# Optimization experiments

Measured on AMD Instinct MI355X. Metric: run time of the kernel, lower is better.

The kernel has to match this reference:

```python
import jax, jax.numpy as jnp
import numpy as np

N_LANGS = 2
VOCAB = 200000
DIM = 300
B = 1024
S = 50
EPS = 1e-5  # BatchNorm1d default eps


def _bn(x):
    # BatchNorm1d(affine=False) in training mode: per-batch stats, biased variance
    return (x - x.mean(axis=0)) / jnp.sqrt(x.var(axis=0) + EPS)


def setup_inputs() -> dict:
    key = jax.random.key(0)
    ks = jax.random.split(key, 16)
    # frozen per-language embedding tables, stacked: [n_langs, vocab, dim]
    tables = jax.random.normal(ks[0], (N_LANGS, VOCAB, DIM), jnp.float32) * 0.1
    tables = tables.at[:, 0, :].set(0.0)  # padding_idx=0 row
    langs_1 = jax.random.randint(ks[1], (B,), 0, N_LANGS, dtype=jnp.int32)
    langs_2 = jax.random.randint(ks[2], (B,), 0, N_LANGS, dtype=jnp.int32)
    sents_1 = jax.random.randint(ks[3], (B, S), 0, VOCAB, dtype=jnp.int64)
    sents_2 = jax.random.randint(ks[4], (B, S), 0, VOCAB, dtype=jnp.int64)
    # lin1/lin2 initialized to identity in the original module
    w1 = jnp.eye(DIM, dtype=jnp.float32)
    b1 = jax.random.uniform(ks[5], (DIM,), jnp.float32, -0.05, 0.05)
    w2 = jnp.eye(DIM, dtype=jnp.float32)
    b2 = jax.random.uniform(ks[6], (DIM,), jnp.float32, -0.05, 0.05)
    w3 = jax.random.normal(ks[7], (400, 901), jnp.float32) * 0.03
    b3 = jax.random.uniform(ks[8], (400,), jnp.float32, -0.03, 0.03)
    w4 = jax.random.normal(ks[9], (100, 400), jnp.float32) * 0.05
    b4 = jax.random.uniform(ks[10], (100,), jnp.float32, -0.05, 0.05)
    w5 = jax.random.normal(ks[11], (1, 100), jnp.float32) * 0.1
    b5 = jax.random.uniform(ks[12], (1,), jnp.float32, -0.1, 0.1)
    return {
        "langs_1": langs_1, "sents_1": sents_1,
        "langs_2": langs_2, "sents_2": sents_2,
        "tables": tables,
        "w1": w1, "b1": b1, "w2": w2, "b2": b2,
        "w3": w3, "b3": b3, "w4": w4, "b4": b4,
        "w5": w5, "b5": b5,
    }


def reference(langs_1, sents_1, langs_2, sents_2, tables,
              w1, b1, w2, b2, w3, b3, w4, b4, w5, b5):
    # batched table-select + embedding lookup + sum-pool (replaces the per-sample loop)
    x1 = tables[langs_1[:, None], sents_1].sum(axis=1)  # [B, 300]
    x2 = tables[langs_2[:, None], sents_2].sum(axis=1)  # [B, 300]

    def enc(x):
        h = jax.nn.relu(_bn(x @ w1.T + b1))
        return jax.nn.relu(_bn(h @ w2.T + b2))

    o1 = enc(x1)
    o2 = enc(x2)
    cor = jnp.sum(o1 * o2, axis=1, keepdims=True)          # [B, 1]
    nxt = jnp.concatenate([o1, o2, jnp.abs(o1 - o2), cor], axis=1)  # [B, 901]
    h = jax.nn.relu(_bn(nxt @ w3.T + b3))                  # [B, 400]
    h = jax.nn.relu(_bn(h @ w4.T + b4))                    # [B, 100]
    score = h @ w5.T + b5                                  # [B, 1]
    prob = jax.nn.sigmoid(score)
    return prob, o1, o2
```

## Files before the change

kernel.cpp:

```cpp
#include <hip/hip_runtime.h>
#include <math.h>

#define EPS 1e-5f
#define INV_N (1.0f / 1024.0f)


typedef _Float16 f16x8 __attribute__((ext_vector_type(8)));
typedef float f32x4 __attribute__((ext_vector_type(4)));

__device__ __forceinline__ _Float16 f2h(float f) { return (_Float16)f; }

static const int STATS_TOTAL = 3400;

__global__ __launch_bounds__(128) void gather_kernel(
    const int* __restrict__ langs1, const int* __restrict__ sents1,
    const int* __restrict__ langs2, const int* __restrict__ sents2,
    const float* __restrict__ tables, _Float16* __restrict__ xb,
    float* __restrict__ stats)
{
    int idx = blockIdx.x, t = threadIdx.x;
    if (idx == 0) {
        for (int i = t; i < STATS_TOTAL; i += 128) stats[i] = 0.f;
    }
    int side = idx >> 10, b = idx & 1023;
    const int* langs = side ? langs2 : langs1;
    const int* sents = side ? sents2 : sents1;
    __shared__ int toks[50];
    if (t < 50) toks[t] = sents[b * 50 + t];
    __syncthreads();
    const float* base = tables + (size_t)langs[b] * (200000ull * 300ull);
    float a0 = 0.f, a1 = 0.f, a2 = 0.f;
    #pragma unroll 5
    for (int s = 0; s < 50; s++) {
        const float* row = base + (size_t)toks[s] * 300;
        a0 += row[t];
        a1 += row[t + 128];
        if (t < 44) a2 += row[t + 256];
    }
    _Float16* xr = xb + (size_t)idx * 320;
    xr[t] = f2h(a0);
    xr[t + 128] = f2h(a1);
    if (t < 64) xr[t + 256] = (t < 44) ? f2h(a2) : (_Float16)0.f;
}

__global__ __launch_bounds__(256) void wcvt_kernel(
    const float* __restrict__ w1, const float* __restrict__ w2,
    const float* __restrict__ w3, const float* __restrict__ w4,
    _Float16* __restrict__ w1b, _Float16* __restrict__ w2b,
    _Float16* __restrict__ w3b, _Float16* __restrict__ w4b)
{
    int i = blockIdx.x * 256 + threadIdx.x;
    if (i < 102400) {
        int r = i / 320, c = i - r * 320;
        w1b[i] = (r < 300 && c < 300) ? f2h(w1[r * 300 + c]) : (_Float16)0.f;
    } else if (i < 204800) {
        int j = i - 102400; int r = j / 320, c = j - r * 320;
        w2b[j] = (r < 300 && c < 300) ? f2h(w2[r * 300 + c]) : (_Float16)0.f;
    } else if (i < 620544) {
        int j = i - 204800; int r = j / 928, c = j - r * 928;
        w3b[j] = (r < 400 && c < 901) ? f2h(w3[r * 901 + c]) : (_Float16)0.f;
    } else if (i < 673792) {
        int j = i - 620544; int r = j / 416, c = j - r * 416;
        w4b[j] = (r < 100 && c < 400) ? f2h(w4[r * 400 + c]) : (_Float16)0.f;
    }
}

__global__ __launch_bounds__(256) void gemm_f16(
    const _Float16* __restrict__ A, const _Float16* __restrict__ W, int ldk,
    const float* __restrict__ bias, float* __restrict__ C, int ldc,
    int N, int kIters, float* __restrict__ sSum, float* __restrict__ sSq,
    int twoSided)
{
    __shared__ __align__(16) _Float16 lsA[2048];
    __shared__ __align__(16) _Float16 lsW[2048];
    int tid = threadIdx.x;
    int r0 = blockIdx.x * 64, c0 = blockIdx.y * 64;
    int lane = tid & 63;
    int wave = tid >> 6;
    int waveR = wave & 1, waveC = wave >> 1;
    int q = lane >> 4, m = lane & 15;

    int srow = tid >> 2, sseg = tid & 3;
    const _Float16* gA = A + (size_t)(r0 + srow) * ldk + sseg * 8;
    const _Float16* gW = W + (size_t)(c0 + srow) * ldk + sseg * 8;
    _Float16* stA = &lsA[sseg * 512 + srow * 8];
    _Float16* stW = &lsW[sseg * 512 + srow * 8];

    int aoff0 = q * 512 + (waveR * 32 + m) * 8;
    int aoff1 = aoff0 + 128;
    int boff0 = q * 512 + (waveC * 32 + m) * 8;
    int boff1 = boff0 + 128;

    f32x4 acc00 = {0.f,0.f,0.f,0.f}, acc01 = {0.f,0.f,0.f,0.f};
    f32x4 acc10 = {0.f,0.f,0.f,0.f}, acc11 = {0.f,0.f,0.f,0.f};

    for (int kt = 0; kt < kIters; kt++) {
        uint4 va = *(const uint4*)gA;
        uint4 vw = *(const uint4*)gW;
        gA += 32; gW += 32;
        __syncthreads();
        *(uint4*)stA = va;
        *(uint4*)stW = vw;
        __syncthreads();
        f16x8 a0 = *(const f16x8*)&lsA[aoff0];
        f16x8 a1 = *(const f16x8*)&lsA[aoff1];
        f16x8 b0 = *(const f16x8*)&lsW[boff0];
        f16x8 b1 = *(const f16x8*)&lsW[boff1];
        acc00 = __builtin_amdgcn_mfma_f32_16x16x32_f16(a0, b0, acc00, 0, 0, 0);
        acc01 = __builtin_amdgcn_mfma_f32_16x16x32_f16(a0, b1, acc01, 0, 0, 0);
        acc10 = __builtin_amdgcn_mfma_f32_16x16x32_f16(a1, b0, acc10, 0, 0, 0);
        acc11 = __builtin_amdgcn_mfma_f32_16x16x32_f16(a1, b1, acc11, 0, 0, 0);
    }

    int side = (twoSided && r0 >= 1024) ? 1 : 0;
    int gc0 = c0 + waveC * 32 + m;
    int gc1 = gc0 + 16;
    float bias0 = (gc0 < N) ? bias[gc0] : 0.f;
    float bias1 = (gc1 < N) ? bias[gc1] : 0.f;
    float colS0 = 0.f, colQ0 = 0.f, colS1 = 0.f, colQ1 = 0.f;
    #pragma unroll
    for (int i = 0; i < 2; i++) {
        f32x4 cv0 = i ? acc10 : acc00;
        f32x4 cv1 = i ? acc11 : acc01;
        #pragma unroll
        for (int r = 0; r < 4; r++) {
            int gr = r0 + waveR * 32 + i * 16 + q * 4 + r;
            if (gc0 < N) {
                float v = cv0[r] + bias0;
                C[(size_t)gr * ldc + gc0] = v;
                colS0 += v; colQ0 += v * v;
            }
            if (gc1 < N) {
                float v = cv1[r] + bias1;
                C[(size_t)gr * ldc + gc1] = v;
                colS1 += v; colQ1 += v * v;
            }
        }
    }
    colS0 += __shfl_down(colS0, 32); colS0 += __shfl_down(colS0, 16);
    colQ0 += __shfl_down(colQ0, 32); colQ0 += __shfl_down(colQ0, 16);
    colS1 += __shfl_down(colS1, 32); colS1 += __shfl_down(colS1, 16);
    colQ1 += __shfl_down(colQ1, 32); colQ1 += __shfl_down(colQ1, 16);
    if (q == 0) {
        if (gc0 < N) {
            atomicAdd(&sSum[side * N + gc0], colS0);
            atomicAdd(&sSq[side * N + gc0], colQ0);
        }
        if (gc1 < N) {
            atomicAdd(&sSum[side * N + gc1], colS1);
            atomicAdd(&sSq[side * N + gc1], colQ1);
        }
    }
}

__global__ __launch_bounds__(256) void bncvt1_kernel(
    const float* __restrict__ z, const float* __restrict__ sS,
    const float* __restrict__ sQ, _Float16* __restrict__ out)
{
    int i = blockIdx.x * 256 + threadIdx.x;
    int r = i / 320, c = i - r * 320;
    _Float16 v = (_Float16)0.f;
    if (c < 300) {
        int side = r >> 10;
        float mean = sS[side * 300 + c] * INV_N;
        float var  = sQ[side * 300 + c] * INV_N - mean * mean;
        float x = (z[r * 300 + c] - mean) * rsqrtf(var + EPS);
        v = f2h(fmaxf(x, 0.f));
    }
    out[i] = v;
}

__global__ __launch_bounds__(256) void bncvt3_kernel(
    const float* __restrict__ z, const float* __restrict__ sS,
    const float* __restrict__ sQ, _Float16* __restrict__ out)
{
    int i = blockIdx.x * 256 + threadIdx.x;
    int r = i / 416, c = i - r * 416;
    _Float16 v = (_Float16)0.f;
    if (c < 400) {
        float mean = sS[c] * INV_N;
        float var  = sQ[c] * INV_N - mean * mean;
        float x = (z[r * 400 + c] - mean) * rsqrtf(var + EPS);
        v = f2h(fmaxf(x, 0.f));
    }
    out[i] = v;
}

__global__ __launch_bounds__(128) void pair_kernel(
    const float* __restrict__ z2, const float* __restrict__ sS,
    const float* __restrict__ sQ, float* __restrict__ out,
    _Float16* __restrict__ nxtb)
{
    int b = blockIdx.x, t = threadIdx.x;
    __shared__ float red[128];
    float dot = 0.f;
    for (int d = t; d < 300; d += 128) {
        float m1 = sS[d] * INV_N;
        float v1 = sQ[d] * INV_N - m1 * m1;
        float m2 = sS[300 + d] * INV_N;
        float v2 = sQ[300 + d] * INV_N - m2 * m2;
        float a1 = fmaxf((z2[(size_t)b * 300 + d] - m1) * rsqrtf(v1 + EPS), 0.f);
        float a2 = fmaxf((z2[(size_t)(1024 + b) * 300 + d] - m2) * rsqrtf(v2 + EPS), 0.f);
        out[1024 + (size_t)b * 300 + d] = a1;
        out[308224 + (size_t)b * 300 + d] = a2;
        nxtb[(size_t)b * 928 + d] = f2h(a1);
        nxtb[(size_t)b * 928 + 300 + d] = f2h(a2);
        nxtb[(size_t)b * 928 + 600 + d] = f2h(fabsf(a1 - a2));
        dot += a1 * a2;
    }
    red[t] = dot;
    __syncthreads();
    if (t < 27) nxtb[(size_t)b * 928 + 901 + t] = (_Float16)0.f;
    if (t == 0) {
        float s = 0.f;
        for (int i = 0; i < 128; i++) s += red[i];
        nxtb[(size_t)b * 928 + 900] = f2h(s);
    }
}

__global__ __launch_bounds__(64) void final_kernel(
    const float* __restrict__ y4, const float* __restrict__ sS,
    const float* __restrict__ sQ, const float* __restrict__ w5,
    const float* __restrict__ b5, float* __restrict__ out)
{
    int b = blockIdx.x, l = threadIdx.x;
    float acc = 0.f;
    for (int j = l; j < 100; j += 64) {
        float mean = sS[j] * INV_N;
        float var = sQ[j] * INV_N - mean * mean;
        float v = (y4[(size_t)b * 100 + j] - mean) * rsqrtf(var + EPS);
        v = v > 0.f ? v : 0.f;
        acc += v * w5[j];
    }
    #pragma unroll
    for (int off = 32; off; off >>= 1) acc += __shfl_down(acc, off);
    if (l == 0) out[b] = 1.f / (1.f + expf(-(acc + b5[0])));
}

extern "C" void kernel_launch(void* const* d_in, const int* in_sizes, int n_in,
                              void* d_out, int out_size, void* d_ws, size_t ws_size,
                              hipStream_t stream)
{
    const int* langs1 = (const int*)d_in[0];
    const int* sents1 = (const int*)d_in[1];
    const int* langs2 = (const int*)d_in[2];
    const int* sents2 = (const int*)d_in[3];
    const float* tables = (const float*)d_in[4];
    const float* w1 = (const float*)d_in[5];
    const float* b1 = (const float*)d_in[6];
    const float* w2 = (const float*)d_in[7];
    const float* b2 = (const float*)d_in[8];
    const float* w3 = (const float*)d_in[9];
    const float* b3 = (const float*)d_in[10];
    const float* w4 = (const float*)d_in[11];
    const float* b4 = (const float*)d_in[12];
    const float* w5 = (const float*)d_in[13];
    const float* b5 = (const float*)d_in[14];

    float* ws = (float*)d_ws;
    float* F0 = ws;
    float* F1 = ws + 614400;
    float* stats = ws + 1228800;
    float* s1S = stats;        float* s1Q = stats + 600;
    float* s2S = stats + 1200; float* s2Q = stats + 1800;
    float* s3S = stats + 2400; float* s3Q = stats + 2800;
    float* s4S = stats + 3200; float* s4Q = stats + 3300;
    _Float16* hb = (_Float16*)(ws + 1232208);
    _Float16* xb   = hb;
    _Float16* a1b  = hb + 655360;
    _Float16* nxtb = hb + 1310720;
    _Float16* a3b  = hb + 2260992;
    _Float16* w1b  = hb + 2686976;
    _Float16* w2b  = hb + 2789376;
    _Float16* w3b  = hb + 2891776;
    _Float16* w4b  = hb + 3307520;

    float* out = (float*)d_out;

    gather_kernel<<<2048, 128, 0, stream>>>(langs1, sents1, langs2, sents2,
                                            tables, xb, stats);
    wcvt_kernel<<<2632, 256, 0, stream>>>(w1, w2, w3, w4, w1b, w2b, w3b, w4b);
    gemm_f16<<<dim3(32, 5), 256, 0, stream>>>(xb, w1b, 320, b1, F0, 300,
                                              300, 10, s1S, s1Q, 1);
    bncvt1_kernel<<<2560, 256, 0, stream>>>(F0, s1S, s1Q, a1b);
    gemm_f16<<<dim3(32, 5), 256, 0, stream>>>(a1b, w2b, 320, b2, F1, 300,
                                              300, 10, s2S, s2Q, 1);
    pair_kernel<<<1024, 128, 0, stream>>>(F1, s2S, s2Q, out, nxtb);
    gemm_f16<<<dim3(16, 7), 256, 0, stream>>>(nxtb, w3b, 928, b3, F0, 400,
                                              400, 29, s3S, s3Q, 0);
    bncvt3_kernel<<<1664, 256, 0, stream>>>(F0, s3S, s3Q, a3b);
    gemm_f16<<<dim3(16, 2), 256, 0, stream>>>(a3b, w4b, 416, b4, F1, 100,
                                              100, 13, s4S, s4Q, 0);
    final_kernel<<<1024, 64, 0, stream>>>(F1, s4S, s4Q, w5, b5, out);
}
```

Before: 644.9 us.

## Fuse all pipeline stages into one cooperative persistent kernel with grid syncs

Replaces the ten separate launches with one cooperative kernel of 256 blocks. The blocks loop over the gather, weight conversion, GEMM tiles, BN/ReLU conversion, pairing and final scoring stages, with grid.sync between stages. The aim is to remove launch overhead and the gaps between dependent kernels. In exchange the latency-bound embedding gather now runs with far fewer resident waves: one 256-thread block per CU that processes samples one after another. Grid-wide barriers also leave idle blocks waiting during the small GEMM stages.

```diff
diff --git a/kernel.cpp b/kernel.cpp
--- a/kernel.cpp
+++ b/kernel.cpp
@@ -1,5 +1,8 @@
 #include <hip/hip_runtime.h>
+#include <hip/hip_cooperative_groups.h>
 #include <math.h>
+
+namespace cg = cooperative_groups;
 
 #define EPS 1e-5f
 #define INV_N (1.0f / 1024.0f)
@@ -10,71 +13,23 @@
 
 __device__ __forceinline__ _Float16 f2h(float f) { return (_Float16)f; }
 
-static const int STATS_TOTAL = 3400;
-
-__global__ __launch_bounds__(128) void gather_kernel(
-    const int* __restrict__ langs1, const int* __restrict__ sents1,
-    const int* __restrict__ langs2, const int* __restrict__ sents2,
-    const float* __restrict__ tables, _Float16* __restrict__ xb,
-    float* __restrict__ stats)
+struct Params {
+    const int *langs1, *sents1, *langs2, *sents2;
+    const float *tables, *w1, *b1, *w2, *b2, *w3, *b3, *w4, *b4, *w5, *b5;
+    float *F0, *F1, *stats, *out;
+    _Float16 *xb, *a1b, *nxtb, *a3b, *w1b, *w2b, *w3b, *w4b;
+};
+
+__device__ void gemm_tile(const _Float16* __restrict__ A,
+                          const _Float16* __restrict__ W, int ldk,
+                          const float* __restrict__ bias,
+                          float* __restrict__ C, int ldc, int N, int kIters,
+                          float* __restrict__ sSum, float* __restrict__ sSq,
+                          int twoSided, int bx, int by,
+                          _Float16* lsA, _Float16* lsW)
 {
-    int idx = blockIdx.x, t = threadIdx.x;
-    if (idx == 0) {
-        for (int i = t; i < STATS_TOTAL; i += 128) stats[i] = 0.f;
-    }
-    int side = idx >> 10, b = idx & 1023;
-    const int* langs = side ? langs2 : langs1;
-    const int* sents = side ? sents2 : sents1;
-    __shared__ int toks[50];
-    if (t < 50) toks[t] = sents[b * 50 + t];
-    __syncthreads();
-    const float* base = tables + (size_t)langs[b] * (200000ull * 300ull);
-    float a0 = 0.f, a1 = 0.f, a2 = 0.f;
-    #pragma unroll 5
-    for (int s = 0; s < 50; s++) {
-        const float* row = base + (size_t)toks[s] * 300;
-        a0 += row[t];
-        a1 += row[t + 128];
-        if (t < 44) a2 += row[t + 256];
-    }
-    _Float16* xr = xb + (size_t)idx * 320;
-    xr[t] = f2h(a0);
-    xr[t + 128] = f2h(a1);
-    if (t < 64) xr[t + 256] = (t < 44) ? f2h(a2) : (_Float16)0.f;
-}
-
-__global__ __launch_bounds__(256) void wcvt_kernel(
-    const float* __restrict__ w1, const float* __restrict__ w2,
-    const float* __restrict__ w3, const float* __restrict__ w4,
-    _Float16* __restrict__ w1b, _Float16* __restrict__ w2b,
-    _Float16* __restrict__ w3b, _Float16* __restrict__ w4b)
-{
-    int i = blockIdx.x * 256 + threadIdx.x;
-    if (i < 102400) {
-        int r = i / 320, c = i - r * 320;
-        w1b[i] = (r < 300 && c < 300) ? f2h(w1[r * 300 + c]) : (_Float16)0.f;
-    } else if (i < 204800) {
-        int j = i - 102400; int r = j / 320, c = j - r * 320;
-        w2b[j] = (r < 300 && c < 300) ? f2h(w2[r * 300 + c]) : (_Float16)0.f;
-    } else if (i < 620544) {
-        int j = i - 204800; int r = j / 928, c = j - r * 928;
-        w3b[j] = (r < 400 && c < 901) ? f2h(w3[r * 901 + c]) : (_Float16)0.f;
-    } else if (i < 673792) {
-        int j = i - 620544; int r = j / 416, c = j - r * 416;
-        w4b[j] = (r < 100 && c < 400) ? f2h(w4[r * 400 + c]) : (_Float16)0.f;
-    }
-}
-
-__global__ __launch_bounds__(256) void gemm_f16(
-    const _Float16* __restrict__ A, const _Float16* __restrict__ W, int ldk,
-    const float* __restrict__ bias, float* __restrict__ C, int ldc,
-    int N, int kIters, float* __restrict__ sSum, float* __restrict__ sSq,
-    int twoSided)
-{
-    __shared__ __align__(16) _Float16 lsA[2048];
-    __shared__ __align__(16) _Float16 lsW[2048];
     int tid = threadIdx.x;
-    int r0 = blockIdx.x * 64, c0 = blockIdx.y * 64;
+    int r0 = bx * 64, c0 = by * 64;
     int lane = tid & 63;
     int wave = tid >> 6;
     int waveR = wave & 1, waveC = wave >> 1;
@@ -153,143 +108,217 @@
     }
 }
 
-__global__ __launch_bounds__(256) void bncvt1_kernel(
-    const float* __restrict__ z, const float* __restrict__ sS,
-    const float* __restrict__ sQ, _Float16* __restrict__ out)
+__global__ __launch_bounds__(256) void fused_kernel(Params p)
 {
-    int i = blockIdx.x * 256 + threadIdx.x;
-    int r = i / 320, c = i - r * 320;
-    _Float16 v = (_Float16)0.f;
-    if (c < 300) {
-        int side = r >> 10;
-        float mean = sS[side * 300 + c] * INV_N;
-        float var  = sQ[side * 300 + c] * INV_N - mean * mean;
-        float x = (z[r * 300 + c] - mean) * rsqrtf(var + EPS);
-        v = f2h(fmaxf(x, 0.f));
-    }
-    out[i] = v;
-}
-
-__global__ __launch_bounds__(256) void bncvt3_kernel(
-    const float* __restrict__ z, const float* __restrict__ sS,
-    const float* __restrict__ sQ, _Float16* __restrict__ out)
-{
-    int i = blockIdx.x * 256 + threadIdx.x;
-    int r = i / 416, c = i - r * 416;
-    _Float16 v = (_Float16)0.f;
-    if (c < 400) {
-        float mean = sS[c] * INV_N;
-        float var  = sQ[c] * INV_N - mean * mean;
-        float x = (z[r * 400 + c] - mean) * rsqrtf(var + EPS);
-        v = f2h(fmaxf(x, 0.f));
-    }
-    out[i] = v;
-}
-
-__global__ __launch_bounds__(128) void pair_kernel(
-    const float* __restrict__ z2, const float* __restrict__ sS,
-    const float* __restrict__ sQ, float* __restrict__ out,
-    _Float16* __restrict__ nxtb)
-{
-    int b = blockIdx.x, t = threadIdx.x;
-    __shared__ float red[128];
-    float dot = 0.f;
-    for (int d = t; d < 300; d += 128) {
-        float m1 = sS[d] * INV_N;
-        float v1 = sQ[d] * INV_N - m1 * m1;
-        float m2 = sS[300 + d] * INV_N;
-        float v2 = sQ[300 + d] * INV_N - m2 * m2;
-        float a1 = fmaxf((z2[(size_t)b * 300 + d] - m1) * rsqrtf(v1 + EPS), 0.f);
-        float a2 = fmaxf((z2[(size_t)(1024 + b) * 300 + d] - m2) * rsqrtf(v2 + EPS), 0.f);
-        out[1024 + (size_t)b * 300 + d] = a1;
-        out[308224 + (size_t)b * 300 + d] = a2;
-        nxtb[(size_t)b * 928 + d] = f2h(a1);
-        nxtb[(size_t)b * 928 + 300 + d] = f2h(a2);
-        nxtb[(size_t)b * 928 + 600 + d] = f2h(fabsf(a1 - a2));
-        dot += a1 * a2;
-    }
-    red[t] = dot;
-    __syncthreads();
-    if (t < 27) nxtb[(size_t)b * 928 + 901 + t] = (_Float16)0.f;
-    if (t == 0) {
-        float s = 0.f;
-        for (int i = 0; i < 128; i++) s += red[i];
-        nxtb[(size_t)b * 928 + 900] = f2h(s);
-    }
-}
-
-__global__ __launch_bounds__(64) void final_kernel(
-    const float* __restrict__ y4, const float* __restrict__ sS,
-    const float* __restrict__ sQ, const float* __restrict__ w5,
-    const float* __restrict__ b5, float* __restrict__ out)
-{
-    int b = blockIdx.x, l = threadIdx.x;
-    float acc = 0.f;
-    for (int j = l; j < 100; j += 64) {
-        float mean = sS[j] * INV_N;
-        float var = sQ[j] * INV_N - mean * mean;
-        float v = (y4[(size_t)b * 100 + j] - mean) * rsqrtf(var + EPS);
-        v = v > 0.f ? v : 0.f;
-        acc += v * w5[j];
-    }
-    #pragma unroll
-    for (int off = 32; off; off >>= 1) acc += __shfl_down(acc, off);
-    if (l == 0) out[b] = 1.f / (1.f + expf(-(acc + b5[0])));
+    cg::grid_group grid = cg::this_grid();
+    __shared__ __align__(16) _Float16 lsA[2048];
+    __shared__ __align__(16) _Float16 lsW[2048];
+    __shared__ float redbuf[8];
+    __shared__ int toks[50];
+
+    const int t = threadIdx.x;
+    const int lane = t & 63, wave = t >> 6;
+    const int bid = blockIdx.x;
+    const int gsz = gridDim.x * 256;
+
+    float* s1S = p.stats;        float* s1Q = p.stats + 600;
+    float* s2S = p.stats + 1200; float* s2Q = p.stats + 1800;
+    float* s3S = p.stats + 2400; float* s3Q = p.stats + 2800;
+    float* s4S = p.stats + 3200; float* s4Q = p.stats + 3300;
+
+    { int i = bid * 256 + t; if (i < 3400) p.stats[i] = 0.f; }
+
+    for (int v = bid; v < 2048; v += gridDim.x) {
+        int side = v >> 10, b = v & 1023;
+        const int* langs = side ? p.langs2 : p.langs1;
+        const int* sents = side ? p.sents2 : p.sents1;
+        __syncthreads();
+        if (t < 50) toks[t] = sents[b * 50 + t];
+        __syncthreads();
+        const float* base = p.tables + (size_t)langs[b] * (200000ull * 300ull);
+        float a0 = 0.f, a1 = 0.f;
+        #pragma unroll 5
+        for (int s = 0; s < 50; s++) {
+            const float* row = base + (size_t)toks[s] * 300;
+            a0 += row[t];
+            if (t < 44) a1 += row[t + 256];
+        }
+        _Float16* xr = p.xb + (size_t)v * 320;
+        xr[t] = f2h(a0);
+        if (t < 64) xr[t + 256] = (t < 44) ? f2h(a1) : (_Float16)0.f;
+    }
+
+    for (int i = bid * 256 + t; i < 673792; i += gsz) {
+        if (i < 102400) {
+            int r = i / 320, c = i - r * 320;
+            p.w1b[i] = (r < 300 && c < 300) ? f2h(p.w1[r * 300 + c]) : (_Float16)0.f;
+        } else if (i < 204800) {
+            int j = i - 102400; int r = j / 320, c = j - r * 320;
+            p.w2b[j] = (r < 300 && c < 300) ? f2h(p.w2[r * 300 + c]) : (_Float16)0.f;
+        } else if (i < 620544) {
+            int j = i - 204800; int r = j / 928, c = j - r * 928;
+            p.w3b[j] = (r < 400 && c < 901) ? f2h(p.w3[r * 901 + c]) : (_Float16)0.f;
+        } else {
+            int j = i - 620544; int r = j / 416, c = j - r * 416;
+            p.w4b[j] = (r < 100 && c < 400) ? f2h(p.w4[r * 400 + c]) : (_Float16)0.f;
+        }
+    }
+    __threadfence();
+    grid.sync();
+
+    if (bid < 160)
+        gemm_tile(p.xb, p.w1b, 320, p.b1, p.F0, 300, 300, 10,
+                  s1S, s1Q, 1, bid & 31, bid >> 5, lsA, lsW);
+    __threadfence();
+    grid.sync();
+
+    for (int i = bid * 256 + t; i < 655360; i += gsz) {
+        int r = i / 320, c = i - r * 320;
+        _Float16 v = (_Float16)0.f;
+        if (c < 300) {
+            int side = r >> 10;
+            float mean = s1S[side * 300 + c] * INV_N;
+            float var  = s1Q[side * 300 + c] * INV_N - mean * mean;
+            float x = (p.F0[r * 300 + c] - mean) * rsqrtf(var + EPS);
+            v = f2h(fmaxf(x, 0.f));
+        }
+        p.a1b[i] = v;
+    }
+    __threadfence();
+    grid.sync();
+
+    if (bid < 160)
+        gemm_tile(p.a1b, p.w2b, 320, p.b2, p.F1, 300, 300, 10,
+                  s2S, s2Q, 1, bid & 31, bid >> 5, lsA, lsW);
+    __threadfence();
+    grid.sync();
+
+    for (int v = bid; v < 1024; v += gridDim.x) {
+        float dot = 0.f;
+        {
+            int d = t;
+            float m1 = s2S[d] * INV_N;
+            float v1 = s2Q[d] * INV_N - m1 * m1;
+            float m2 = s2S[300 + d] * INV_N;
+            float v2 = s2Q[300 + d] * INV_N - m2 * m2;
+            float a1 = fmaxf((p.F1[(size_t)v * 300 + d] - m1) * rsqrtf(v1 + EPS), 0.f);
+            float a2 = fmaxf((p.F1[(size_t)(1024 + v) * 300 + d] - m2) * rsqrtf(v2 + EPS), 0.f);
+            p.out[1024 + (size_t)v * 300 + d] = a1;
+            p.out[308224 + (size_t)v * 300 + d] = a2;
+            p.nxtb[(size_t)v * 928 + d] = f2h(a1);
+            p.nxtb[(size_t)v * 928 + 300 + d] = f2h(a2);
+            p.nxtb[(size_t)v * 928 + 600 + d] = f2h(fabsf(a1 - a2));
+            dot += a1 * a2;
+        }
+        if (t < 44) {
+            int d = t + 256;
+            float m1 = s2S[d] * INV_N;
+            float v1 = s2Q[d] * INV_N - m1 * m1;
+            float m2 = s2S[300 + d] * INV_N;
+            float v2 = s2Q[300 + d] * INV_N - m2 * m2;
+            float a1 = fmaxf((p.F1[(size_t)v * 300 + d] - m1) * rsqrtf(v1 + EPS), 0.f);
+            float a2 = fmaxf((p.F1[(size_t)(1024 + v) * 300 + d] - m2) * rsqrtf(v2 + EPS), 0.f);
+            p.out[1024 + (size_t)v * 300 + d] = a1;
+            p.out[308224 + (size_t)v * 300 + d] = a2;
+            p.nxtb[(size_t)v * 928 + d] = f2h(a1);
+            p.nxtb[(size_t)v * 928 + 300 + d] = f2h(a2);
+            p.nxtb[(size_t)v * 928 + 600 + d] = f2h(fabsf(a1 - a2));
+            dot += a1 * a2;
+        }
+        #pragma unroll
+        for (int off = 32; off; off >>= 1) dot += __shfl_down(dot, off);
+        __syncthreads();
+        if (lane == 0) redbuf[wave] = dot;
+        __syncthreads();
+        if (t == 0)
+            p.nxtb[(size_t)v * 928 + 900] =
+                f2h(redbuf[0] + redbuf[1] + redbuf[2] + redbuf[3]);
+        if (t < 27) p.nxtb[(size_t)v * 928 + 901 + t] = (_Float16)0.f;
+    }
+    __threadfence();
+    grid.sync();
+
+    if (bid < 112)
+        gemm_tile(p.nxtb, p.w3b, 928, p.b3, p.F0, 400, 400, 29,
+                  s3S, s3Q, 0, bid & 15, bid >> 4, lsA, lsW);
+    __threadfence();
+    grid.sync();
+
+    for (int i = bid * 256 + t; i < 425984; i += gsz) {
+        int r = i / 416, c = i - r * 416;
+        _Float16 v = (_Float16)0.f;
+        if (c < 400) {
+            float mean = s3S[c] * INV_N;
+            float var  = s3Q[c] * INV_N - mean * mean;
+            float x = (p.F0[r * 400 + c] - mean) * rsqrtf(var + EPS);
+            v = f2h(fmaxf(x, 0.f));
+        }
+        p.a3b[i] = v;
+    }
+    __threadfence();
+    grid.sync();
+
+    if (bid < 32)
+        gemm_tile(p.a3b, p.w4b, 416, p.b4, p.F1, 100, 100, 13,
+                  s4S, s4Q, 0, bid & 15, bid >> 4, lsA, lsW);
+    __threadfence();
+    grid.sync();
+
+    {
+        int r = bid * 4 + wave;
+        float acc = 0.f;
+        {
+            int j = lane;
+            float mean = s4S[j] * INV_N;
+            float var  = s4Q[j] * INV_N - mean * mean;
+            float v = (p.F1[(size_t)r * 100 + j] - mean) * rsqrtf(var + EPS);
+            acc += fmaxf(v, 0.f) * p.w5[j];
+        }
+        if (lane < 36) {
+            int j = lane + 64;
+            float mean = s4S[j] * INV_N;
+            float var  = s4Q[j] * INV_N - mean * mean;
+            float v = (p.F1[(size_t)r * 100 + j] - mean) * rsqrtf(var + EPS);
+            acc += fmaxf(v, 0.f) * p.w5[j];
+        }
+        #pragma unroll
+        for (int off = 32; off; off >>= 1) acc += __shfl_down(acc, off);
+        if (lane == 0) p.out[r] = 1.f / (1.f + expf(-(acc + p.b5[0])));
+    }
 }
 
 extern "C" void kernel_launch(void* const* d_in, const int* in_sizes, int n_in,
                               void* d_out, int out_size, void* d_ws, size_t ws_size,
                               hipStream_t stream)
 {
-    const int* langs1 = (const int*)d_in[0];
-    const int* sents1 = (const int*)d_in[1];
-    const int* langs2 = (const int*)d_in[2];
-    const int* sents2 = (const int*)d_in[3];
-    const float* tables = (const float*)d_in[4];
-    const float* w1 = (const float*)d_in[5];
-    const float* b1 = (const float*)d_in[6];
-    const float* w2 = (const float*)d_in[7];
-    const float* b2 = (const float*)d_in[8];
-    const float* w3 = (const float*)d_in[9];
-    const float* b3 = (const float*)d_in[10];
-    const float* w4 = (const float*)d_in[11];
-    const float* b4 = (const float*)d_in[12];
-    const float* w5 = (const float*)d_in[13];
-    const float* b5 = (const float*)d_in[14];
-
     float* ws = (float*)d_ws;
-    float* F0 = ws;
-    float* F1 = ws + 614400;
-    float* stats = ws + 1228800;
-    float* s1S = stats;        float* s1Q = stats + 600;
-    float* s2S = stats + 1200; float* s2Q = stats + 1800;
-    float* s3S = stats + 2400; float* s3Q = stats + 2800;
-    float* s4S = stats + 3200; float* s4Q = stats + 3300;
     _Float16* hb = (_Float16*)(ws + 1232208);
-    _Float16* xb   = hb;
-    _Float16* a1b  = hb + 655360;
-    _Float16* nxtb = hb + 1310720;
-    _Float16* a3b  = hb + 2260992;
-    _Float16* w1b  = hb + 2686976;
-    _Float16* w2b  = hb + 2789376;
-    _Float16* w3b  = hb + 2891776;
-    _Float16* w4b  = hb + 3307520;
-
-    float* out = (float*)d_out;
-
-    gather_kernel<<<2048, 128, 0, stream>>>(langs1, sents1, langs2, sents2,
-                                            tables, xb, stats);
-    wcvt_kernel<<<2632, 256, 0, stream>>>(w1, w2, w3, w4, w1b, w2b, w3b, w4b);
-    gemm_f16<<<dim3(32, 5), 256, 0, stream>>>(xb, w1b, 320, b1, F0, 300,
-                                              300, 10, s1S, s1Q, 1);
-    bncvt1_kernel<<<2560, 256, 0, stream>>>(F0, s1S, s1Q, a1b);
-    gemm_f16<<<dim3(32, 5), 256, 0, stream>>>(a1b, w2b, 320, b2, F1, 300,
-                                              300, 10, s2S, s2Q, 1);
-    pair_kernel<<<1024, 128, 0, stream>>>(F1, s2S, s2Q, out, nxtb);
-    gemm_f16<<<dim3(16, 7), 256, 0, stream>>>(nxtb, w3b, 928, b3, F0, 400,
-                                              400, 29, s3S, s3Q, 0);
-    bncvt3_kernel<<<1664, 256, 0, stream>>>(F0, s3S, s3Q, a3b);
-    gemm_f16<<<dim3(16, 2), 256, 0, stream>>>(a3b, w4b, 416, b4, F1, 100,
-                                              100, 13, s4S, s4Q, 0);
-    final_kernel<<<1024, 64, 0, stream>>>(F1, s4S, s4Q, w5, b5, out);
+
+    Params p;
+    p.langs1 = (const int*)d_in[0];
+    p.sents1 = (const int*)d_in[1];
+    p.langs2 = (const int*)d_in[2];
+    p.sents2 = (const int*)d_in[3];
+    p.tables = (const float*)d_in[4];
+    p.w1 = (const float*)d_in[5];  p.b1 = (const float*)d_in[6];
+    p.w2 = (const float*)d_in[7];  p.b2 = (const float*)d_in[8];
+    p.w3 = (const float*)d_in[9];  p.b3 = (const float*)d_in[10];
+    p.w4 = (const float*)d_in[11]; p.b4 = (const float*)d_in[12];
+    p.w5 = (const float*)d_in[13]; p.b5 = (const float*)d_in[14];
+    p.F0 = ws;
+    p.F1 = ws + 614400;
+    p.stats = ws + 1228800;
+    p.out = (float*)d_out;
+    p.xb   = hb;
+    p.a1b  = hb + 655360;
+    p.nxtb = hb + 1310720;
+    p.a3b  = hb + 2260992;
+    p.w1b  = hb + 2686976;
+    p.w2b  = hb + 2789376;
+    p.w3b  = hb + 2891776;
+    p.w4b  = hb + 3307520;
+
+    void* args[] = { &p };
+    hipLaunchCooperativeKernel(reinterpret_cast<void*>(fused_kernel),
+                               dim3(256), dim3(256), args, 0, stream);
 }
```

Measured after the change: 1.209 ms. 1.87x slower.
